# Kernel tuning notes

Hardware: AMD Instinct MI355X
Metric: run time of the kernel (lower is better)

The kernel has to match this reference:

```python
import jax, jax.numpy as jnp
import numpy as np

N = 100000      # nodes
E = 1600000     # edges
IN = 128        # in_channels
H = 128         # hidden_channels
OUT = 40        # out_channels
EPS = 1e-5      # BatchNorm eps


def setup_inputs() -> dict:
    key = jax.random.key(0)
    ks = jax.random.split(key, 16)
    s_in = 1.0 / np.sqrt(IN)
    s_h = 1.0 / np.sqrt(H)
    s_fc = 1.0 / np.sqrt(IN + 2 * H)
    return {
        "x": jax.random.normal(ks[0], (N, IN), dtype=jnp.float32),
        "edge_index": jax.random.randint(ks[1], (2, E), 0, N, dtype=jnp.int32),
        "W1": jax.random.normal(ks[2], (IN, H), dtype=jnp.float32) * s_in,
        "b1": jnp.zeros((H,), dtype=jnp.float32),
        "W2": jax.random.normal(ks[3], (H, H), dtype=jnp.float32) * s_h,
        "b2": jnp.zeros((H,), dtype=jnp.float32),
        "bn1_gamma": jnp.ones((H,), dtype=jnp.float32),
        "bn1_beta": jnp.zeros((H,), dtype=jnp.float32),
        "bn1_mean": jax.random.normal(ks[4], (H,), dtype=jnp.float32) * 0.1,
        "bn1_var": jax.random.uniform(ks[5], (H,), dtype=jnp.float32, minval=0.5, maxval=1.5),
        "bn2_gamma": jnp.ones((H,), dtype=jnp.float32),
        "bn2_beta": jnp.zeros((H,), dtype=jnp.float32),
        "bn2_mean": jax.random.normal(ks[6], (H,), dtype=jnp.float32) * 0.1,
        "bn2_var": jax.random.uniform(ks[7], (H,), dtype=jnp.float32, minval=0.5, maxval=1.5),
        "fc_W": jax.random.normal(ks[8], (IN + 2 * H, OUT), dtype=jnp.float32) * s_fc,
        "fc_b": jnp.zeros((OUT,), dtype=jnp.float32),
    }


def _gcn_conv(x, edge_index, W, b):
    """PyG GCNConv: symmetric norm with self-loops. x:[N,F_in] -> [N,F_out]."""
    row, col = edge_index[0], edge_index[1]  # messages flow col -> row
    h = x @ W                                 # [N, F_out] transform first
    deg = jax.ops.segment_sum(jnp.ones((E,), x.dtype), row, num_segments=N) + 1.0  # +1 self-loop
    dinv = jax.lax.rsqrt(deg)                 # deg^{-1/2}
    norm = dinv[row] * dinv[col]              # [E]
    msg = h[col] * norm[:, None]              # gather + scale
    agg = jax.ops.segment_sum(msg, row, num_segments=N)
    agg = agg + h * (dinv * dinv)[:, None]    # self-loop contribution
    return agg + b


def _bn_eval(x, gamma, beta, mean, var):
    return (x - mean) * (gamma * jax.lax.rsqrt(var + EPS)) + beta


def reference(x, edge_index, W1, b1, W2, b2,
              bn1_gamma, bn1_beta, bn1_mean, bn1_var,
              bn2_gamma, bn2_beta, bn2_mean, bn2_var,
              fc_W, fc_b):
    x0 = x
    x1 = _gcn_conv(x0, edge_index, W1, b1)
    x1 = jax.nn.relu(_bn_eval(x1, bn1_gamma, bn1_beta, bn1_mean, bn1_var))
    # dropout: eval mode -> identity
    x2 = _gcn_conv(x1, edge_index, W2, b2)
    x2 = jax.nn.relu(_bn_eval(x2, bn2_gamma, bn2_beta, bn2_mean, bn2_var))
    out = jnp.concatenate([x0, x1, x2], axis=-1) @ fc_W + fc_b  # [N, OUT]
    return out
```

## Files before the change

kernel.cpp:

```cpp
#include <hip/hip_runtime.h>

#define N_NODES 100000
#define N_EDGES 1600000
#define C_H     128
#define C_OUT   40
#define K_FC    384
#define BN_EPS  1e-5f
#define NB      391
#define CHUNK   6144

typedef unsigned int uint;

__global__ void zero_i32(int* p, int n) {
    int i = blockIdx.x * blockDim.x + threadIdx.x;
    if (i < n) p[i] = 0;
}

__global__ __launch_bounds__(256) void bucket_count(const int* __restrict__ erow,
                                                    int* __restrict__ bcnt) {
    __shared__ int cnt[NB];
    for (int i = threadIdx.x; i < NB; i += 256) cnt[i] = 0;
    __syncthreads();
    const int c0 = blockIdx.x * CHUNK;
    const int c1 = min(c0 + CHUNK, N_EDGES);
    for (int e = c0 + threadIdx.x; e < c1; e += 256)
        atomicAdd(&cnt[erow[e] >> 8], 1);
    __syncthreads();
    for (int i = threadIdx.x; i < NB; i += 256)
        if (cnt[i]) atomicAdd(&bcnt[i], cnt[i]);
}

__global__ __launch_bounds__(256) void scan_buckets(const int* __restrict__ bcnt,
                                                    int* __restrict__ bstart,
                                                    int* __restrict__ bfill) {
    __shared__ int sa[512], sb[512];
    const int t = threadIdx.x;
    int v0 = (t < NB) ? bcnt[t] : 0;
    int v1 = (t + 256 < NB) ? bcnt[t + 256] : 0;
    sa[t] = v0; sa[t + 256] = v1;
    __syncthreads();
    int* src = sa; int* dst = sb;
    for (int off = 1; off < 512; off <<= 1) {
        dst[t]       = src[t]       + (t >= off ? src[t - off] : 0);
        dst[t + 256] = src[t + 256] + (t + 256 >= off ? src[t + 256 - off] : 0);
        __syncthreads();
        int* tmp = src; src = dst; dst = tmp;
    }
    if (t < NB)       { bstart[t] = src[t] - v0;             bfill[t] = src[t] - v0; }
    if (t + 256 < NB) { bstart[t + 256] = src[t + 256] - v1; bfill[t + 256] = src[t + 256] - v1; }
    if (t == 0) bstart[NB] = N_EDGES;
}

__global__ __launch_bounds__(256) void bucket_bin(const int* __restrict__ erow,
                                                  const int* __restrict__ ecol,
                                                  int* __restrict__ bfill,
                                                  int2* __restrict__ pairs) {
    __shared__ int cnt[NB];
    __shared__ int lpos[NB];
    for (int i = threadIdx.x; i < NB; i += 256) cnt[i] = 0;
    __syncthreads();
    const int c0 = blockIdx.x * CHUNK;
    const int c1 = min(c0 + CHUNK, N_EDGES);
    for (int e = c0 + threadIdx.x; e < c1; e += 256)
        atomicAdd(&cnt[erow[e] >> 8], 1);
    __syncthreads();
    for (int i = threadIdx.x; i < NB; i += 256)
        lpos[i] = cnt[i] ? atomicAdd(&bfill[i], cnt[i]) : 0;
    __syncthreads();
    for (int e = c0 + threadIdx.x; e < c1; e += 256) {
        int r = erow[e], c = ecol[e];
        int p = atomicAdd(&lpos[r >> 8], 1);
        pairs[p] = make_int2(r, c);
    }
}

__global__ __launch_bounds__(256) void bucket_csr(const int2* __restrict__ pairs,
                                                  const int* __restrict__ bstart,
                                                  int* __restrict__ rowptr,
                                                  float* __restrict__ dinv,
                                                  int* __restrict__ colsg) {
    __shared__ int lcnt[256], sa[256], sb[256], lpos[256];
    const int b = blockIdx.x;
    const int t = threadIdx.x;
    const int p0 = bstart[b], p1 = bstart[b + 1];
    lcnt[t] = 0;
    __syncthreads();
    for (int i = p0 + t; i < p1; i += 256)
        atomicAdd(&lcnt[pairs[i].x & 255], 1);
    __syncthreads();
    sa[t] = lcnt[t];
    __syncthreads();
    int* src = sa; int* dst = sb;
    for (int off = 1; off < 256; off <<= 1) {
        dst[t] = src[t] + (t >= off ? src[t - off] : 0);
        __syncthreads();
        int* tmp = src; src = dst; dst = tmp;
    }
    const int excl = src[t] - lcnt[t];
    const int r = b * 256 + t;
    if (r < N_NODES) {
        rowptr[r] = p0 + excl;
        dinv[r] = rsqrtf((float)lcnt[t] + 1.0f);
    }
    if (b == NB - 1 && t == 0) rowptr[N_NODES] = N_EDGES;
    lpos[t] = excl;
    __syncthreads();
    for (int i = p0 + t; i < p1; i += 256) {
        int2 pr = pairs[i];
        int s = atomicAdd(&lpos[pr.x & 255], 1);
        colsg[p0 + s] = pr.y;
    }
}

__global__ void bn_coef(const float* b1, const float* g1, const float* be1,
                        const float* m1, const float* v1,
                        const float* b2, const float* g2, const float* be2,
                        const float* m2, const float* v2,
                        float* s1, float* t1, float* s2, float* t2) {
    int f = threadIdx.x;
    float sa = g1[f] * rsqrtf(v1[f] + BN_EPS);
    s1[f] = sa;
    t1[f] = (b1[f] - m1[f]) * sa + be1[f];
    float sb = g2[f] * rsqrtf(v2[f] + BN_EPS);
    s2[f] = sb;
    t2[f] = (b2[f] - m2[f]) * sb + be2[f];
}

#define FMA4(A, S, V) \
    A.x = fmaf(S, V.x, A.x); A.y = fmaf(S, V.y, A.y); \
    A.z = fmaf(S, V.z, A.z); A.w = fmaf(S, V.w, A.w);

__device__ inline uint pack_bf16x2(float a, float b) {
    uint ua = __builtin_bit_cast(uint, a);
    uint ub = __builtin_bit_cast(uint, b);
    ua += 0x7fffu + ((ua >> 16) & 1u);
    ub += 0x7fffu + ((ub >> 16) & 1u);
    return (ua >> 16) | (ub & 0xffff0000u);
}

__global__ __launch_bounds__(256) void gemm_scaled(const float* __restrict__ X,
                                                   const float* __restrict__ W,
                                                   const float* __restrict__ dinv,
                                                   uint* __restrict__ Hs) {
    __shared__ float wl[64 * 128];
    __shared__ float xl[32 * 68];

    const int tid = threadIdx.x;
    const int rg = tid >> 5;
    const int c4 = (tid & 31) << 2;
    const int rb = blockIdx.x * 32;
    const int r0 = rb + rg * 4;

    float4 acc0 = {0,0,0,0}, acc1 = {0,0,0,0}, acc2 = {0,0,0,0}, acc3 = {0,0,0,0};

    for (int half = 0; half < 2; ++half) {
        const int k0 = half * 64;
        __syncthreads();
        {
            const float4* W4 = (const float4*)(W + (size_t)k0 * 128);
            float4* wl4 = (float4*)wl;
            #pragma unroll
            for (int i = 0; i < 8; ++i) wl4[tid + i * 256] = W4[tid + i * 256];
        }
        #pragma unroll
        for (int i = 0; i < 2; ++i) {
            int f = tid + i * 256;
            int row = f >> 4, cc = f & 15;
            float4 v = *(const float4*)(X + (size_t)(rb + row) * 128 + k0 + cc * 4);
            *(float4*)&xl[row * 68 + cc * 4] = v;
        }
        __syncthreads();

        for (int k4 = 0; k4 < 16; ++k4) {
            const float* wr = wl + k4 * 4 * 128 + c4;
            float4 w0 = *(const float4*)(wr);
            float4 w1 = *(const float4*)(wr + 128);
            float4 w2 = *(const float4*)(wr + 256);
            float4 w3 = *(const float4*)(wr + 384);
            float4 xv0 = *(const float4*)&xl[(rg * 4 + 0) * 68 + k4 * 4];
            float4 xv1 = *(const float4*)&xl[(rg * 4 + 1) * 68 + k4 * 4];
            float4 xv2 = *(const float4*)&xl[(rg * 4 + 2) * 68 + k4 * 4];
            float4 xv3 = *(const float4*)&xl[(rg * 4 + 3) * 68 + k4 * 4];
            FMA4(acc0, xv0.x, w0) FMA4(acc0, xv0.y, w1) FMA4(acc0, xv0.z, w2) FMA4(acc0, xv0.w, w3)
            FMA4(acc1, xv1.x, w0) FMA4(acc1, xv1.y, w1) FMA4(acc1, xv1.z, w2) FMA4(acc1, xv1.w, w3)
            FMA4(acc2, xv2.x, w0) FMA4(acc2, xv2.y, w1) FMA4(acc2, xv2.z, w2) FMA4(acc2, xv2.w, w3)
            FMA4(acc3, xv3.x, w0) FMA4(acc3, xv3.y, w1) FMA4(acc3, xv3.z, w2) FMA4(acc3, xv3.w, w3)
        }
    }
    float d0 = dinv[r0], d1 = dinv[r0 + 1], d2 = dinv[r0 + 2], d3 = dinv[r0 + 3];
    uint2 o;
    o.x = pack_bf16x2(acc0.x * d0, acc0.y * d0);
    o.y = pack_bf16x2(acc0.z * d0, acc0.w * d0);
    *(uint2*)(Hs + (size_t)(r0 + 0) * 64 + (c4 >> 1)) = o;
    o.x = pack_bf16x2(acc1.x * d1, acc1.y * d1);
    o.y = pack_bf16x2(acc1.z * d1, acc1.w * d1);
    *(uint2*)(Hs + (size_t)(r0 + 1) * 64 + (c4 >> 1)) = o;
    o.x = pack_bf16x2(acc2.x * d2, acc2.y * d2);
    o.y = pack_bf16x2(acc2.z * d2, acc2.w * d2);
    *(uint2*)(Hs + (size_t)(r0 + 2) * 64 + (c4 >> 1)) = o;
    o.x = pack_bf16x2(acc3.x * d3, acc3.y * d3);
    o.y = pack_bf16x2(acc3.z * d3, acc3.w * d3);
    *(uint2*)(Hs + (size_t)(r0 + 3) * 64 + (c4 >> 1)) = o;
}

#define ACC1(V) \
    accx += __builtin_bit_cast(float, V << 16); \
    accy += __builtin_bit_cast(float, V & 0xffff0000u);

__global__ __launch_bounds__(256) void spmm_bn_relu4(
    const uint* __restrict__ Hs, const int* __restrict__ cols,
    const int* __restrict__ rowptr, const float* __restrict__ dinv,
    const float* __restrict__ s, const float* __restrict__ t,
    float* __restrict__ Y) {
    const int lane = threadIdx.x & 63;
    const int r = blockIdx.x * 4 + (threadIdx.x >> 6);

    uint vself = Hs[(size_t)r * 64 + lane];
    float accx = __builtin_bit_cast(float, vself << 16);
    float accy = __builtin_bit_cast(float, vself & 0xffff0000u);
    const float di = dinv[r];
    const int e0 = rowptr[r], e1 = rowptr[r + 1];
    int j = e0;
    const int n16 = e0 + ((e1 - e0) & ~15);
    for (; j < n16; j += 16) {
        uint v[16];
        #pragma unroll
        for (int q = 0; q < 16; ++q)
            v[q] = Hs[(size_t)cols[j + q] * 64 + lane];
        #pragma unroll
        for (int q = 0; q < 16; ++q) { ACC1(v[q]) }
    }
    const int n4 = e0 + ((e1 - e0) & ~3);
    for (; j < n4; j += 4) {
        uint v[4];
        #pragma unroll
        for (int q = 0; q < 4; ++q)
            v[q] = Hs[(size_t)cols[j + q] * 64 + lane];
        #pragma unroll
        for (int q = 0; q < 4; ++q) { ACC1(v[q]) }
    }
    for (; j < e1; ++j) {
        uint v0 = Hs[(size_t)cols[j] * 64 + lane];
        ACC1(v0)
    }
    float2 sf = ((const float2*)s)[lane];
    float2 tf = ((const float2*)t)[lane];
    float2 o;
    o.x = fmaxf(fmaf(accx * di, sf.x, tf.x), 0.0f);
    o.y = fmaxf(fmaf(accy * di, sf.y, tf.y), 0.0f);
    ((float2*)Y)[(size_t)r * 64 + lane] = o;
}

__global__ __launch_bounds__(256) void final_gemm6(
    const float* __restrict__ X0, const float* __restrict__ X1,
    const float* __restrict__ X2, const float* __restrict__ fcW,
    const float* __restrict__ fcb, float* __restrict__ out) {
    __shared__ float xs[2][128 * 17];
    __shared__ float wt[2][640];

    const int t = threadIdx.x;
    const int lane = t & 63;
    const int w = t >> 6;
    const int rbase = blockIdx.x * 128;

    float acc[2][10];
    #pragma unroll
    for (int rr = 0; rr < 2; ++rr)
        #pragma unroll
        for (int c = 0; c < 10; ++c) acc[rr][c] = 0.0f;

    const float* segs[3] = {X0, X1, X2};

    float4 xr[2];
    float wr[3];

    auto load_chunk = [&](int ch) {
        const int k0 = ch * 16;
        const float* xseg = segs[k0 >> 7];
        const int koff = k0 & 127;
        #pragma unroll
        for (int i = 0; i < 2; ++i) {
            int f = t + i * 256;
            int row = f >> 2, cc = f & 3;
            int r = rbase + row;
            float4 v = {0, 0, 0, 0};
            if (r < N_NODES)
                v = *(const float4*)(xseg + (size_t)r * 128 + koff + cc * 4);
            xr[i] = v;
        }
        #pragma unroll
        for (int i = 0; i < 3; ++i) {
            int idx = t + i * 256;
            float v = 0.0f;
            if (idx < 640) {
                int c = idx >> 4, kk = idx & 15;
                v = fcW[(size_t)(k0 + kk) * 40 + c];
            }
            wr[i] = v;
        }
    };

    auto store_chunk = [&](int buf) {
        #pragma unroll
        for (int i = 0; i < 2; ++i) {
            int f = t + i * 256;
            int row = f >> 2, cc = f & 3;
            xs[buf][row * 17 + cc * 4 + 0] = xr[i].x;
            xs[buf][row * 17 + cc * 4 + 1] = xr[i].y;
            xs[buf][row * 17 + cc * 4 + 2] = xr[i].z;
            xs[buf][row * 17 + cc * 4 + 3] = xr[i].w;
        }
        #pragma unroll
        for (int i = 0; i < 3; ++i) {
            int idx = t + i * 256;
            if (idx < 640) wt[buf][idx] = wr[i];
        }
    };

    load_chunk(0);
    for (int ch = 0; ch < 24; ++ch) {
        const int buf = ch & 1;
        store_chunk(buf);
        if (ch < 23) load_chunk(ch + 1);
        __syncthreads();
        #pragma unroll
        for (int kk4 = 0; kk4 < 4; ++kk4) {
            float4 wv[10];
            #pragma unroll
            for (int c = 0; c < 10; ++c)
                wv[c] = *(const float4*)&wt[buf][(w * 10 + c) * 16 + kk4 * 4];
            #pragma unroll
            for (int i = 0; i < 4; ++i) {
                float xa = xs[buf][(lane) * 17 + kk4 * 4 + i];
                float xb = xs[buf][(64 + lane) * 17 + kk4 * 4 + i];
                #pragma unroll
                for (int c = 0; c < 10; ++c) {
                    float wc = (i == 0) ? wv[c].x : (i == 1) ? wv[c].y
                             : (i == 2) ? wv[c].z : wv[c].w;
                    acc[0][c] = fmaf(xa, wc, acc[0][c]);
                    acc[1][c] = fmaf(xb, wc, acc[1][c]);
                }
            }
        }
    }

    #pragma unroll
    for (int rr = 0; rr < 2; ++rr) {
        int r = rbase + rr * 64 + lane;
        if (r < N_NODES) {
            #pragma unroll
            for (int c2 = 0; c2 < 5; ++c2) {
                float2 o;
                o.x = acc[rr][c2 * 2 + 0] + fcb[w * 10 + c2 * 2 + 0];
                o.y = acc[rr][c2 * 2 + 1] + fcb[w * 10 + c2 * 2 + 1];
                *(float2*)(out + (size_t)r * 40 + w * 10 + c2 * 2) = o;
            }
        }
    }
}

extern "C" void kernel_launch(void* const* d_in, const int* in_sizes, int n_in,
                              void* d_out, int out_size, void* d_ws, size_t ws_size,
                              hipStream_t stream) {
    const float* x   = (const float*)d_in[0];
    const int*   ei  = (const int*)d_in[1];
    const int* e_row = ei;
    const int* e_col = ei + N_EDGES;
    const float* W1  = (const float*)d_in[2];
    const float* b1  = (const float*)d_in[3];
    const float* W2  = (const float*)d_in[4];
    const float* b2  = (const float*)d_in[5];
    const float* g1  = (const float*)d_in[6];
    const float* be1 = (const float*)d_in[7];
    const float* m1  = (const float*)d_in[8];
    const float* v1  = (const float*)d_in[9];
    const float* g2  = (const float*)d_in[10];
    const float* be2 = (const float*)d_in[11];
    const float* m2  = (const float*)d_in[12];
    const float* v2  = (const float*)d_in[13];
    const float* fcW = (const float*)d_in[14];
    const float* fcb = (const float*)d_in[15];
    float* out = (float*)d_out;

    char* ws = (char*)d_ws;
    size_t off = 0;
    auto alloc = [&](size_t b) {
        char* p = ws + off;
        off += (b + 255) & ~(size_t)255;
        return p;
    };
    uint*  h      = (uint*)alloc((size_t)N_NODES * C_H * 2);
    float* x1     = (float*)alloc((size_t)N_NODES * C_H * 4);
    float* x2     = (float*)alloc((size_t)N_NODES * C_H * 4);
    int2*  pairs  = (int2*)alloc((size_t)N_EDGES * 8);
    int*   cols   = (int*)alloc((size_t)N_EDGES * 4);
    float* dinv   = (float*)alloc(N_NODES * 4);
    int*   rowptr = (int*)alloc((N_NODES + 1) * 4);
    int*   bcnt   = (int*)alloc((NB + 1) * 4);
    int*   bstart = (int*)alloc((NB + 1) * 4);
    int*   bfill  = (int*)alloc((NB + 1) * 4);
    float* coef   = (float*)alloc(512 * 4);
    float* s1 = coef, *t1 = coef + 128, *s2 = coef + 256, *t2 = coef + 384;

    const int nwg_bin = (N_EDGES + CHUNK - 1) / CHUNK;

    zero_i32<<<2, 256, 0, stream>>>(bcnt, NB);
    bucket_count<<<nwg_bin, 256, 0, stream>>>(e_row, bcnt);
    scan_buckets<<<1, 256, 0, stream>>>(bcnt, bstart, bfill);
    bucket_bin<<<nwg_bin, 256, 0, stream>>>(e_row, e_col, bfill, pairs);
    bucket_csr<<<NB, 256, 0, stream>>>(pairs, bstart, rowptr, dinv, cols);
    bn_coef<<<1, 128, 0, stream>>>(b1, g1, be1, m1, v1, b2, g2, be2, m2, v2,
                                   s1, t1, s2, t2);

    gemm_scaled<<<N_NODES / 32, 256, 0, stream>>>(x, W1, dinv, h);
    spmm_bn_relu4<<<N_NODES / 4, 256, 0, stream>>>(h, cols, rowptr, dinv, s1, t1, x1);
    gemm_scaled<<<N_NODES / 32, 256, 0, stream>>>(x1, W2, dinv, h);
    spmm_bn_relu4<<<N_NODES / 4, 256, 0, stream>>>(h, cols, rowptr, dinv, s2, t2, x2);
    final_gemm6<<<(N_NODES + 127) / 128, 256, 0, stream>>>(x, x1, x2, fcW, fcb, out);
}
```

Measured before the change: 515.4 us.

## Read FC weights as wave-uniform scalar loads and shrink row tile to 64

The final GEMM no longer stages fc weights in LDS. Each wave reads its 10 output columns straight from global memory through a readfirstlane-uniform pointer, so the loads can become scalar loads. The row tile drops from 128 to 64 with 32-wide K chunks, so each thread keeps one row of 10 accumulators and there are twice as many blocks. This removes LDS weight traffic and its bank conflicts. In exchange each weight is reused across only 64 rows per block and the scalar loads depend on the scalar cache.

Result: no change. 519.1 us (+0.7%).

```diff
diff --git a/kernel.cpp b/kernel.cpp
--- a/kernel.cpp
+++ b/kernel.cpp
@@ -251,110 +251,81 @@
     ((float2*)Y)[(size_t)r * 64 + lane] = o;
 }
 
-__global__ __launch_bounds__(256) void final_gemm6(
+__global__ __launch_bounds__(256) void final_gemm7(
     const float* __restrict__ X0, const float* __restrict__ X1,
     const float* __restrict__ X2, const float* __restrict__ fcW,
     const float* __restrict__ fcb, float* __restrict__ out) {
-    __shared__ float xs[2][128 * 17];
-    __shared__ float wt[2][640];
+    __shared__ float xs[2][64 * 33];
 
     const int t = threadIdx.x;
     const int lane = t & 63;
-    const int w = t >> 6;
-    const int rbase = blockIdx.x * 128;
-
-    float acc[2][10];
+    const int wq = __builtin_amdgcn_readfirstlane(t >> 6);
+    const float* wbase = fcW + wq * 10;
+    const int rbase = blockIdx.x * 64;
+
+    float acc[10];
     #pragma unroll
-    for (int rr = 0; rr < 2; ++rr)
-        #pragma unroll
-        for (int c = 0; c < 10; ++c) acc[rr][c] = 0.0f;
+    for (int c = 0; c < 10; ++c) acc[c] = 0.0f;
 
     const float* segs[3] = {X0, X1, X2};
-
     float4 xr[2];
-    float wr[3];
 
     auto load_chunk = [&](int ch) {
-        const int k0 = ch * 16;
-        const float* xseg = segs[k0 >> 7];
-        const int koff = k0 & 127;
+        const float* xseg = segs[ch >> 2];
+        const int koff = (ch & 3) * 32;
         #pragma unroll
         for (int i = 0; i < 2; ++i) {
             int f = t + i * 256;
-            int row = f >> 2, cc = f & 3;
+            int row = f >> 3, cc = f & 7;
             int r = rbase + row;
             float4 v = {0, 0, 0, 0};
             if (r < N_NODES)
                 v = *(const float4*)(xseg + (size_t)r * 128 + koff + cc * 4);
             xr[i] = v;
         }
-        #pragma unroll
-        for (int i = 0; i < 3; ++i) {
-            int idx = t + i * 256;
-            float v = 0.0f;
-            if (idx < 640) {
-                int c = idx >> 4, kk = idx & 15;
-                v = fcW[(size_t)(k0 + kk) * 40 + c];
-            }
-            wr[i] = v;
-        }
     };
 
     auto store_chunk = [&](int buf) {
         #pragma unroll
         for (int i = 0; i < 2; ++i) {
             int f = t + i * 256;
-            int row = f >> 2, cc = f & 3;
-            xs[buf][row * 17 + cc * 4 + 0] = xr[i].x;
-            xs[buf][row * 17 + cc * 4 + 1] = xr[i].y;
-            xs[buf][row * 17 + cc * 4 + 2] = xr[i].z;
-            xs[buf][row * 17 + cc * 4 + 3] = xr[i].w;
-        }
-        #pragma unroll
-        for (int i = 0; i < 3; ++i) {
-            int idx = t + i * 256;
-            if (idx < 640) wt[buf][idx] = wr[i];
+            int row = f >> 3, cc = f & 7;
+            float* p = &xs[buf][row * 33 + cc * 4];
+            p[0] = xr[i].x; p[1] = xr[i].y; p[2] = xr[i].z; p[3] = xr[i].w;
         }
     };
 
     load_chunk(0);
-    for (int ch = 0; ch < 24; ++ch) {
+    for (int ch = 0; ch < 12; ++ch) {
         const int buf = ch & 1;
         store_chunk(buf);
-        if (ch < 23) load_chunk(ch + 1);
-        __syncthreads();
-        #pragma unroll
-        for (int kk4 = 0; kk4 < 4; ++kk4) {
-            float4 wv[10];
+        if (ch < 11) load_chunk(ch + 1);
+        __syncthreads();
+        const int k0 = ch * 32;
+        #pragma unroll
+        for (int kk4 = 0; kk4 < 8; ++kk4) {
+            float xv[4];
             #pragma unroll
-            for (int c = 0; c < 10; ++c)
-                wv[c] = *(const float4*)&wt[buf][(w * 10 + c) * 16 + kk4 * 4];
+            for (int j = 0; j < 4; ++j)
+                xv[j] = xs[buf][lane * 33 + kk4 * 4 + j];
             #pragma unroll
-            for (int i = 0; i < 4; ++i) {
-                float xa = xs[buf][(lane) * 17 + kk4 * 4 + i];
-                float xb = xs[buf][(64 + lane) * 17 + kk4 * 4 + i];
+            for (int j = 0; j < 4; ++j) {
+                const float* wr = wbase + (size_t)(k0 + kk4 * 4 + j) * 40;
                 #pragma unroll
-                for (int c = 0; c < 10; ++c) {
-                    float wc = (i == 0) ? wv[c].x : (i == 1) ? wv[c].y
-                             : (i == 2) ? wv[c].z : wv[c].w;
-                    acc[0][c] = fmaf(xa, wc, acc[0][c]);
-                    acc[1][c] = fmaf(xb, wc, acc[1][c]);
-                }
+                for (int c = 0; c < 10; ++c)
+                    acc[c] = fmaf(xv[j], wr[c], acc[c]);
             }
         }
     }
 
-    #pragma unroll
-    for (int rr = 0; rr < 2; ++rr) {
-        int r = rbase + rr * 64 + lane;
-        if (r < N_NODES) {
-            #pragma unroll
-            for (int c2 = 0; c2 < 5; ++c2) {
-                float2 o;
-                o.x = acc[rr][c2 * 2 + 0] + fcb[w * 10 + c2 * 2 + 0];
-                o.y = acc[rr][c2 * 2 + 1] + fcb[w * 10 + c2 * 2 + 1];
-                *(float2*)(out + (size_t)r * 40 + w * 10 + c2 * 2) = o;
-            }
+    const int r = rbase + lane;
+    if (r < N_NODES) {
+        #pragma unroll
+        for (int c2 = 0; c2 < 5; ++c2) {
+            float2 o;
+            o.x = acc[c2 * 2 + 0] + fcb[wq * 10 + c2 * 2 + 0];
+            o.y = acc[c2 * 2 + 1] + fcb[wq * 10 + c2 * 2 + 1];
+            *(float2*)(out + (size_t)r * 40 + wq * 10 + c2 * 2) = o;
         }
     }
 }
@@ -416,5 +387,5 @@
     spmm_bn_relu4<<<N_NODES / 4, 256, 0, stream>>>(h, cols, rowptr, dinv, s1, t1, x1);
     gemm_scaled<<<N_NODES / 32, 256, 0, stream>>>(x1, W2, dinv, h);
     spmm_bn_relu4<<<N_NODES / 4, 256, 0, stream>>>(h, cols, rowptr, dinv, s2, t2, x2);
-    final_gemm6<<<(N_NODES + 127) / 128, 256, 0, stream>>>(x, x1, x2, fcW, fcb, out);
-}
+    final_gemm7<<<(N_NODES + 63) / 64, 256, 0, stream>>>(x, x1, x2, fcW, fcb, out);
+}
```
